# Kernel tuning notes

Hardware: AMD Instinct MI355X
Metric: run time of the kernel (lower is better)

## Reference

```python
import jax, jax.numpy as jnp
import numpy as np

B, N, D, H = 128, 197, 384, 1536  # batch, patches+CLS, embed_dim, hidden_dim


def _layer_norm(x, g, b, eps=1e-5):
    m = jnp.mean(x, axis=-1, keepdims=True)
    v = jnp.mean(jnp.square(x - m), axis=-1, keepdims=True)
    return (x - m) * jax.lax.rsqrt(v + eps) * g + b


def setup_inputs() -> dict:
    key = jax.random.key(0)
    ks = jax.random.split(key, 8)
    x = jax.random.normal(ks[0], (B, N, D), dtype=jnp.float32)
    # quantum circuit surrogates: orthogonal-style square matrices
    V = jax.random.normal(ks[1], (D, D), dtype=jnp.float32) / np.sqrt(D)
    W = jax.random.normal(ks[2], (D, D), dtype=jnp.float32) / np.sqrt(D)
    ln1_g = jnp.ones((D,), jnp.float32); ln1_b = jnp.zeros((D,), jnp.float32)
    ln2_g = jnp.ones((D,), jnp.float32); ln2_b = jnp.zeros((D,), jnp.float32)
    W1 = jax.random.normal(ks[3], (D, H), dtype=jnp.float32) / np.sqrt(D)
    b1 = jnp.zeros((H,), jnp.float32)
    W2 = jax.random.normal(ks[4], (H, D), dtype=jnp.float32) / np.sqrt(H)
    b2 = jnp.zeros((D,), jnp.float32)
    return {"x": x, "ln1_g": ln1_g, "ln1_b": ln1_b, "V": V, "W": W,
            "ln2_g": ln2_g, "ln2_b": ln2_b, "W1": W1, "b1": b1, "W2": W2, "b2": b2}


def reference(x, ln1_g, ln1_b, V, W, ln2_g, ln2_b, W1, b1, W2, b2):
    inp = _layer_norm(x, ln1_g, ln1_b)
    # normalization across the patch axis (dim=1), exactly as in the torch code
    inp = inp / jnp.sqrt(jnp.sum(jnp.square(inp) + 1e-4, axis=1, keepdims=True) + 1e-8)
    # Vx circuit: unary-basis probabilities |(V x_i)_d|^2 -> vx[b, d, i]
    vx = jnp.square(jnp.einsum('de,bne->bdn', V, inp))            # [B, D, N]
    # xWx circuit: (x_i^T W x_j)^2 -> xwx[b, i, j]
    y = jnp.einsum('bnd,de->bne', inp, W)                         # [B, N, D]
    xwx = jnp.square(jnp.einsum('bne,bme->bnm', y, inp))          # [B, N, N]
    vx = jnp.sqrt(vx + 1e-8)
    xwx = jnp.sqrt(xwx + 1e-8)
    attn = jax.nn.softmax(xwx, axis=-1)                           # [B, N, N]
    t = jnp.einsum('bnm,bdm->bnd', attn, vx)                      # attn @ vx^T
    x = x + t
    h = _layer_norm(x, ln2_g, ln2_b)
    h = jax.nn.gelu(h @ W1 + b1) @ W2 + b2                        # dropout=0 (eval)
    return x + h
```

## Files before the change

### kernel.cpp

```cpp
#include <hip/hip_runtime.h>
#include <math.h>

typedef unsigned short u16;
typedef unsigned int u32;
typedef __bf16 bfv8 __attribute__((ext_vector_type(8)));
typedef float f32x4 __attribute__((ext_vector_type(4)));

#define BB 128
#define NN 197
#define DD 384
#define HH 1536
#define BN (BB*NN)
#define NP 224

__device__ __forceinline__ float bf2f(u16 h){ u32 u = ((u32)h)<<16; float f; __builtin_memcpy(&f,&u,4); return f; }
__device__ __forceinline__ u16 f2bf(float x){ u32 u; __builtin_memcpy(&u,&x,4); u = (u + 0x7fffu + ((u>>16)&1u))>>16; return (u16)u; }

__device__ __forceinline__ float fast_gelu(float z){
  float t2 = 1.5957691216f*z*(1.f + 0.044715f*z*z);
  return z * __builtin_amdgcn_rcpf(1.f + __expf(-t2));
}

__device__ __forceinline__ void gload16(const void* g, void* s){
  __builtin_amdgcn_global_load_lds(
      (const __attribute__((address_space(1))) void*)g,
      (__attribute__((address_space(3))) void*)s, 16, 0, 0);
}

#define WAITV(N) asm volatile("s_waitcnt vmcnt(" #N ")" ::: "memory")

__global__ __launch_bounds__(256) void ln1_stats(const float* __restrict__ x,
    float* __restrict__ mu, float* __restrict__ rv){
  int row = blockIdx.x*4 + (threadIdx.x>>6);
  int lane = threadIdx.x & 63;
  const float* xr = x + (long)row*DD;
  float s=0.f, ss=0.f;
  #pragma unroll
  for (int j=0;j<DD/64;j++){ float v = xr[lane + j*64]; s+=v; ss+=v*v; }
  #pragma unroll
  for (int m=32;m;m>>=1){ s += __shfl_xor(s,m); ss += __shfl_xor(ss,m); }
  if (lane==0){
    float mn = s*(1.f/DD);
    float var = ss*(1.f/DD) - mn*mn;
    mu[row]=mn; rv[row]=1.f/sqrtf(var+1e-5f);
  }
}

__global__ __launch_bounds__(256) void colnorm(const float* __restrict__ x,
    const float* __restrict__ mu, const float* __restrict__ rv,
    const float* __restrict__ g, const float* __restrict__ bt,
    float* __restrict__ scale){
  int i = blockIdx.x*256 + threadIdx.x;
  int b = i/DD, d = i - b*DD;
  const float* xp = x + (long)b*NN*DD + d;
  float gd = g[d], bd = bt[d];
  float s = 0.f;
  for (int n=0;n<NN;n++){
    float v = (xp[(long)n*DD] - mu[b*NN+n]) * rv[b*NN+n] * gd + bd;
    s += v*v;
  }
  scale[i] = 1.f/sqrtf(s + 197.f*1e-4f + 1e-8f);
}

__global__ __launch_bounds__(256) void ln_apply(const float* __restrict__ x,
    const float* __restrict__ mu, const float* __restrict__ rv,
    const float* __restrict__ g, const float* __restrict__ bt,
    const float* __restrict__ scale, u16* __restrict__ inpn){
  long i = (long)blockIdx.x*256 + threadIdx.x;
  int d = (int)(i % DD);
  long row = i / DD;
  int b = (int)(row / NN);
  float v = (x[i]-mu[row])*rv[row]*g[d]+bt[d];
  inpn[i] = f2bf(v * scale[b*DD+d]);
}

__global__ __launch_bounds__(256) void prep_weights(const float* __restrict__ V, const float* __restrict__ W,
    const float* __restrict__ W1, const float* __restrict__ W2,
    u16* __restrict__ Vb, u16* __restrict__ Wt, u16* __restrict__ W1t, u16* __restrict__ W2t){
  int i = blockIdx.x*256 + threadIdx.x;
  if (i < DD*DD){
    Vb[i] = f2bf(V[i]);
    int r = i/DD, c = i - r*DD;
    Wt[c*DD + r] = f2bf(W[i]);
  }
  {
    int r = i/HH, c = i - r*HH;
    W1t[(long)c*DD + r] = f2bf(W1[i]);
    int r2 = i/DD, c2 = i - r2*DD;
    W2t[(long)c2*HH + r2] = f2bf(W2[i]);
  }
}

__global__ __launch_bounds__(256) void transpose_pad(const u16* __restrict__ U, u16* __restrict__ Ut){
  __shared__ u16 tile[32][33];
  int b = blockIdx.x, dt = blockIdx.y, pt = blockIdx.z;
  int tx = threadIdx.x & 31, ty = threadIdx.x >> 5;
  const u16* Ub = U + (long)b*NN*DD;
  #pragma unroll
  for (int j=0;j<4;j++){
    int p = pt*32 + ty + j*8;
    int d = dt*32 + tx;
    tile[ty+j*8][tx] = (p<NN) ? Ub[(long)p*DD + d] : (u16)0;
  }
  __syncthreads();
  u16* Utb = Ut + (long)b*DD*NP;
  #pragma unroll
  for (int j=0;j<4;j++){
    int d = dt*32 + ty + j*8;
    int p = pt*32 + tx;
    Utb[(long)d*NP + p] = tile[tx][ty+j*8];
  }
}

__global__ __launch_bounds__(256) void softmax_rows(const u16* __restrict__ S, u16* __restrict__ attn){
  int row = blockIdx.x*4 + (threadIdx.x>>6);
  int lane = threadIdx.x & 63;
  const u16* sr = S + (long)row*NP;
  float v[4]; float mx = -1e30f;
  #pragma unroll
  for (int j=0;j<4;j++){ int c = lane + j*64; v[j] = (c<NN)? bf2f(sr[c]) : -1e30f; mx = fmaxf(mx, v[j]); }
  #pragma unroll
  for (int m=32;m;m>>=1) mx = fmaxf(mx, __shfl_xor(mx,m));
  float sm = 0.f;
  #pragma unroll
  for (int j=0;j<4;j++){ v[j] = __expf(v[j]-mx); sm += v[j]; }
  #pragma unroll
  for (int m=32;m;m>>=1) sm += __shfl_xor(sm,m);
  float inv = __builtin_amdgcn_rcpf(sm);
  u16* ar = attn + (long)row*NP;
  #pragma unroll
  for (int j=0;j<4;j++){ int c = lane + j*64; if (c<NP) ar[c] = f2bf(v[j]*inv); }
}

__global__ __launch_bounds__(256) void ln2_fused(const u16* __restrict__ x2,
    const float* __restrict__ g, const float* __restrict__ bt, u16* __restrict__ h){
  int row = blockIdx.x*4 + (threadIdx.x>>6);
  int lane = threadIdx.x & 63;
  const u16* xr = x2 + (long)row*DD;
  float v[6]; float s=0.f, ss=0.f;
  #pragma unroll
  for (int j=0;j<6;j++){ v[j]=bf2f(xr[lane+j*64]); s+=v[j]; ss+=v[j]*v[j]; }
  #pragma unroll
  for (int m=32;m;m>>=1){ s+=__shfl_xor(s,m); ss+=__shfl_xor(ss,m); }
  float mn = s*(1.f/DD);
  float rvv = 1.f/sqrtf(ss*(1.f/DD)-mn*mn+1e-5f);
  u16* hr = h + (long)row*DD;
  #pragma unroll
  for (int j=0;j<6;j++){ int d = lane+j*64; hr[d] = f2bf((v[j]-mn)*rvv*g[d]+bt[d]); }
}

struct EpiS { u16* s;
  __device__ void operator()(int b, int r0, int c, const f32x4* col, int mf) const {
    u16* sp = s + ((long)b*NN + r0)*NP + c;
    for (int m=0;m<mf;m++)
      #pragma unroll
      for (int i=0;i<4;i++){
        int r = r0 + m*16 + i;
        float v = col[m][i];
        if (r < NN) sp[(long)(m*16+i)*NP] = f2bf(sqrtf(v*v + 1e-8f));
      }
  }};
struct EpiX2 { u16* x2; const float* x;
  __device__ void operator()(int b, int r0, int c, const f32x4* col, int mf) const {
    long base = ((long)b*NN + r0)*DD + c;
    for (int m=0;m<mf;m++)
      #pragma unroll
      for (int i=0;i<4;i++){
        int r = r0 + m*16 + i;
        if (r < NN){ long idx = base + (long)(m*16+i)*DD; x2[idx] = f2bf(x[idx] + col[m][i]); }
      }
  }};
struct EpiGelu { u16* g; const float* b1;
  __device__ void operator()(int, int r0, int c, const f32x4* col, int mf) const {
    float bb = b1[c];
    u16* gp = g + (long)r0*HH + c;
    for (int m=0;m<mf;m++)
      #pragma unroll
      for (int i=0;i<4;i++)
        gp[(long)(m*16+i)*HH] = f2bf(fast_gelu(col[m][i] + bb));
  }};
struct EpiOut { float* o; const u16* x2; const float* b2;
  __device__ void operator()(int, int r0, int c, const f32x4* col, int mf) const {
    float bb = b2[c];
    long base = (long)r0*DD + c;
    for (int m=0;m<mf;m++)
      #pragma unroll
      for (int i=0;i<4;i++){
        long idx = base + (long)(m*16+i)*DD;
        o[idx] = bf2f(x2[idx]) + col[m][i] + bb;
      }
  }};

template<int BM, class Epi>
__global__ __launch_bounds__(256) void gemm_nt(const u16* __restrict__ A, const u16* __restrict__ B,
    int M, int N, int K, int lda, int ldb, long sA, long sB, int NT, Epi epi)
{
  constexpr int MF = BM/32;
  constexpr int ALOADS = BM/64;
  __shared__ __align__(16) u16 As[2][BM*32];
  __shared__ __align__(16) u16 Bs[2][128*32];
  int wg;
  { int flat = blockIdx.x, nwg = gridDim.x;
    int xcd = flat & 7, local = flat >> 3;
    int q = nwg >> 3, r = nwg & 7;
    wg = (xcd < r ? xcd*(q+1) : r*(q+1) + (xcd-r)*q) + local; }
  const int bm = wg / NT, bn = wg - bm*NT;
  const int bat = blockIdx.y;
  const u16* Ab = A + (long)bat*sA;
  const u16* Bb = B + (long)bat*sB;
  const int t = threadIdx.x, lane = t&63, wid = t>>6, wr = wid>>1, wc = wid&1;
  const int row0 = bm*BM, col0 = bn*128;

  long aoff[ALOADS]; int asoff[ALOADS];
  #pragma unroll
  for (int i=0;i<ALOADS;i++){
    int ob = (i*256+t)*16;
    int r = ob>>6, ke = (ob&63)>>1;
    int ra = row0+r; if (ra>M-1) ra=M-1;
    aoff[i] = (long)ra*lda + ke; asoff[i] = ob;
  }
  long boff[2]; int bsoff[2];
  #pragma unroll
  for (int i=0;i<2;i++){
    int ob = (i*256+t)*16;
    int r = ob>>6, ke = (ob&63)>>1;
    int rb = col0+r; if (rb>N-1) rb=N-1;
    boff[i] = (long)rb*ldb + ke; bsoff[i] = ob;
  }

  auto stage = [&](int buf, int k0){
    #pragma unroll
    for (int i=0;i<ALOADS;i++) gload16(Ab + aoff[i] + k0, (char*)As[buf] + asoff[i]);
    #pragma unroll
    for (int i=0;i<2;i++)      gload16(Bb + boff[i] + k0, (char*)Bs[buf] + bsoff[i]);
  };

  f32x4 acc[MF][4] = {};
  const int kg = (lane>>4)*8, rl = lane&15;
  const int ntile = K/32;

  stage(0, 0);
  stage(1, 32);
  int buf = 0;
  for (int tt=0; tt<ntile; ++tt){
    if (tt+1 < ntile){
      if constexpr (ALOADS == 1) WAITV(3); else WAITV(4);
    } else {
      WAITV(0);
    }
    __builtin_amdgcn_sched_barrier(0);
    __builtin_amdgcn_s_barrier();

    bfv8 af[MF], bfr[4];
    #pragma unroll
    for (int m=0;m<MF;m++) af[m]  = *(const bfv8*)&As[buf][(wr*(BM/2) + m*16 + rl)*32 + kg];
    #pragma unroll
    for (int n=0;n<4;n++)  bfr[n] = *(const bfv8*)&Bs[buf][(wc*64 + n*16 + rl)*32 + kg];
    #pragma unroll
    for (int m=0;m<MF;m++)
      #pragma unroll
      for (int n=0;n<4;n++)
        acc[m][n] = __builtin_amdgcn_mfma_f32_16x16x32_bf16(af[m], bfr[n], acc[m][n], 0,0,0);

    __builtin_amdgcn_s_barrier();
    __builtin_amdgcn_sched_barrier(0);
    if (tt+2 < ntile) stage(buf, (tt+2)*32);
    buf ^= 1;
  }

  const int rbase = row0 + wr*(BM/2) + (lane>>4)*4;
  const int cbase = col0 + wc*64 + rl;
  #pragma unroll
  for (int n=0;n<4;n++){
    int c = cbase + n*16;
    if (c < N){
      f32x4 colv[MF];
      #pragma unroll
      for (int m=0;m<MF;m++) colv[m] = acc[m][n];
      epi(bat, rbase, c, colv, MF);
    }
  }
}

__global__ __launch_bounds__(256) void gemm12(const u16* __restrict__ A,
    const u16* __restrict__ B1, const u16* __restrict__ B2,
    u16* __restrict__ U, u16* __restrict__ Y)
{
  __shared__ __align__(16) u16 As[2][64*32];
  __shared__ __align__(16) u16 B1s[2][128*32];
  __shared__ __align__(16) u16 B2s[2][128*32];
  int wg;
  { int flat = blockIdx.x, nwg = gridDim.x;
    int xcd = flat & 7, local = flat >> 3;
    int q = nwg >> 3, r = nwg & 7;
    wg = (xcd < r ? xcd*(q+1) : r*(q+1) + (xcd-r)*q) + local; }
  const int bm = wg/3, bn = wg - bm*3;
  const int t = threadIdx.x, lane = t&63, wid = t>>6, wr = wid>>1, wc = wid&1;
  const int row0 = bm*64, col0 = bn*128;

  int ob = t*16, r = ob>>6, ke = (ob&63)>>1;
  long aoff = (long)(row0+r)*DD + ke;
  int asoff = ob;
  long boff[2]; int bsoff[2];
  #pragma unroll
  for (int i=0;i<2;i++){
    int ob2 = (i*256+t)*16, r2 = ob2>>6, ke2 = (ob2&63)>>1;
    boff[i] = (long)(col0+r2)*DD + ke2; bsoff[i] = ob2;
  }

  auto stage = [&](int buf, int k0){
    gload16(A + aoff + k0, (char*)As[buf] + asoff);
    #pragma unroll
    for (int i=0;i<2;i++){
      gload16(B1 + boff[i] + k0, (char*)B1s[buf] + bsoff[i]);
      gload16(B2 + boff[i] + k0, (char*)B2s[buf] + bsoff[i]);
    }
  };

  f32x4 acc1[2][4] = {}, acc2[2][4] = {};
  const int kg = (lane>>4)*8, rl = lane&15;

  stage(0, 0);
  stage(1, 32);
  int buf = 0;
  for (int tt=0; tt<12; ++tt){
    if (tt < 11) WAITV(5); else WAITV(0);
    __builtin_amdgcn_sched_barrier(0);
    __builtin_amdgcn_s_barrier();

    bfv8 af[2], b1r[4], b2r[4];
    #pragma unroll
    for (int m=0;m<2;m++) af[m] = *(const bfv8*)&As[buf][(wr*32 + m*16 + rl)*32 + kg];
    #pragma unroll
    for (int n=0;n<4;n++){
      b1r[n] = *(const bfv8*)&B1s[buf][(wc*64 + n*16 + rl)*32 + kg];
      b2r[n] = *(const bfv8*)&B2s[buf][(wc*64 + n*16 + rl)*32 + kg];
    }
    #pragma unroll
    for (int m=0;m<2;m++)
      #pragma unroll
      for (int n=0;n<4;n++){
        acc1[m][n] = __builtin_amdgcn_mfma_f32_16x16x32_bf16(af[m], b1r[n], acc1[m][n], 0,0,0);
        acc2[m][n] = __builtin_amdgcn_mfma_f32_16x16x32_bf16(af[m], b2r[n], acc2[m][n], 0,0,0);
      }

    __builtin_amdgcn_s_barrier();
    __builtin_amdgcn_sched_barrier(0);
    if (tt+2 < 12) stage(buf, (tt+2)*32);
    buf ^= 1;
  }

  const int rbase = row0 + wr*32 + (lane>>4)*4;
  const int cbase = col0 + wc*64 + rl;
  #pragma unroll
  for (int n=0;n<4;n++){
    int c = cbase + n*16;
    #pragma unroll
    for (int m=0;m<2;m++)
      #pragma unroll
      for (int i=0;i<4;i++){
        long idx = (long)(rbase + m*16 + i)*DD + c;
        float v1 = acc1[m][n][i];
        U[idx] = f2bf(sqrtf(v1*v1 + 1e-8f));
        Y[idx] = f2bf(acc2[m][n][i]);
      }
  }
}

extern "C" void kernel_launch(void* const* d_in, const int* in_sizes, int n_in,
                              void* d_out, int out_size, void* d_ws, size_t ws_size,
                              hipStream_t stream){
  const float* x     = (const float*)d_in[0];
  const float* g1    = (const float*)d_in[1];
  const float* b1n   = (const float*)d_in[2];
  const float* V     = (const float*)d_in[3];
  const float* W     = (const float*)d_in[4];
  const float* g2    = (const float*)d_in[5];
  const float* b2n   = (const float*)d_in[6];
  const float* W1    = (const float*)d_in[7];
  const float* bias1 = (const float*)d_in[8];
  const float* W2    = (const float*)d_in[9];
  const float* bias2 = (const float*)d_in[10];
  float* out = (float*)d_out;

  char* ws = (char*)d_ws;
  size_t off = 0;
  auto take = [&](size_t bytes)->char*{ char* p = ws + off; off += (bytes + 255) & ~(size_t)255; return p; };

  float* mu    = (float*)take((size_t)BN*4);
  float* rv    = (float*)take((size_t)BN*4);
  float* scale = (float*)take((size_t)BB*DD*4);
  char* aliasBase = ws + off;
  u16*  inpn = (u16*) take((size_t)BN*DD*2);
  u16*  U    = (u16*) take((size_t)BN*DD*2);
  u16*  Ut   = (u16*) take((size_t)BB*DD*NP*2);
  u16*  Yb   = (u16*) take((size_t)BN*DD*2);
  u16*  S    = (u16*) take((size_t)BN*NP*2);
  u16*  attn = (u16*) take((size_t)BN*NP*2);
  u16*  x2   = (u16*) take((size_t)BN*DD*2);
  u16*  h    = (u16*) take((size_t)BN*DD*2);
  u16*  Vb   = (u16*) take((size_t)DD*DD*2);
  u16*  Wt   = (u16*) take((size_t)DD*DD*2);
  u16*  W1t  = (u16*) take((size_t)DD*HH*2);
  u16*  W2t  = (u16*) take((size_t)DD*HH*2);
  u16*  G    = (u16*)aliasBase;

  prep_weights<<<DD*HH/256, 256, 0, stream>>>(V, W, W1, W2, Vb, Wt, W1t, W2t);
  ln1_stats  <<<BN/4,       256, 0, stream>>>(x, mu, rv);
  colnorm    <<<BB*DD/256,  256, 0, stream>>>(x, mu, rv, g1, b1n, scale);
  ln_apply   <<<BN*DD/256,  256, 0, stream>>>(x, mu, rv, g1, b1n, scale, inpn);

  gemm12<<<394*3, 256, 0, stream>>>(inpn, Vb, Wt, U, Yb);
  { dim3 grid(BB, DD/32, NP/32);
    transpose_pad<<<grid, 256, 0, stream>>>(U, Ut); }
  { dim3 grid(4*2, BB);
    gemm_nt<64,EpiS><<<grid,256,0,stream>>>(Yb, inpn, NN, NN, DD, DD, DD,
                                         (long)NN*DD, (long)NN*DD, 2, EpiS{S}); }
  softmax_rows<<<BN/4, 256, 0, stream>>>(S, attn);
  { dim3 grid(4*3, BB);
    gemm_nt<64,EpiX2><<<grid,256,0,stream>>>(attn, Ut, NN, DD, NP, NP, NP,
                                          (long)NN*NP, (long)DD*NP, 3, EpiX2{x2, x}); }
  ln2_fused<<<BN/4, 256, 0, stream>>>(x2, g2, b2n, h);
  { dim3 grid(197*12, 1);
    gemm_nt<128,EpiGelu><<<grid,256,0,stream>>>(h, W1t, BN, HH, DD, DD, DD, 0, 0, 12, EpiGelu{G, bias1}); }
  { dim3 grid(394*3, 1);
    gemm_nt<64,EpiOut><<<grid,256,0,stream>>>(G, W2t, BN, DD, HH, HH, HH, 0, 0, 3, EpiOut{out, x2, bias2}); }
}
```

Baseline: 395.1 us.

## Stage GELU GEMM output through LDS for coalesced stores; tile weight transposes

Adds a dedicated FC1 GEMM kernel that writes bias+GELU results into a 128x128 LDS tile and then stores them to global memory as 16-byte row-contiguous vectors. The previous epilogue wrote scattered 2-byte values with a row stride. The weight preparation is also split into a plain cast plus shared-memory tiled transpose kernels, so the transposed weight writes are coalesced. The extra 32KB of LDS per block may reduce occupancy, and the weight prep now takes several launches instead of one.

```diff
diff --git a/kernel.cpp b/kernel.cpp
--- a/kernel.cpp
+++ b/kernel.cpp
@@ -5,6 +5,7 @@
 typedef unsigned int u32;
 typedef __bf16 bfv8 __attribute__((ext_vector_type(8)));
 typedef float f32x4 __attribute__((ext_vector_type(4)));
+typedef u16 u16v8 __attribute__((ext_vector_type(8)));
 
 #define BB 128
 #define NN 197
@@ -74,21 +75,23 @@
   inpn[i] = f2bf(v * scale[b*DD+d]);
 }
 
-__global__ __launch_bounds__(256) void prep_weights(const float* __restrict__ V, const float* __restrict__ W,
-    const float* __restrict__ W1, const float* __restrict__ W2,
-    u16* __restrict__ Vb, u16* __restrict__ Wt, u16* __restrict__ W1t, u16* __restrict__ W2t){
+__global__ __launch_bounds__(256) void cast_bf16(const float* __restrict__ src, u16* __restrict__ dst, int n){
   int i = blockIdx.x*256 + threadIdx.x;
-  if (i < DD*DD){
-    Vb[i] = f2bf(V[i]);
-    int r = i/DD, c = i - r*DD;
-    Wt[c*DD + r] = f2bf(W[i]);
-  }
-  {
-    int r = i/HH, c = i - r*HH;
-    W1t[(long)c*DD + r] = f2bf(W1[i]);
-    int r2 = i/DD, c2 = i - r2*DD;
-    W2t[(long)c2*HH + r2] = f2bf(W2[i]);
-  }
+  if (i < n) dst[i] = f2bf(src[i]);
+}
+
+__global__ __launch_bounds__(256) void transpose_cast(const float* __restrict__ src, u16* __restrict__ dst,
+    int R, int C){
+  __shared__ float tile[32][33];
+  int rt = blockIdx.x, ct = blockIdx.y;
+  int tx = threadIdx.x & 31, ty = threadIdx.x >> 5;
+  #pragma unroll
+  for (int j=0;j<4;j++)
+    tile[ty+j*8][tx] = src[(long)(rt*32+ty+j*8)*C + ct*32+tx];
+  __syncthreads();
+  #pragma unroll
+  for (int j=0;j<4;j++)
+    dst[(long)(ct*32+ty+j*8)*R + rt*32+tx] = f2bf(tile[tx][ty+j*8]);
 }
 
 __global__ __launch_bounds__(256) void transpose_pad(const u16* __restrict__ U, u16* __restrict__ Ut){
@@ -169,15 +172,6 @@
         int r = r0 + m*16 + i;
         if (r < NN){ long idx = base + (long)(m*16+i)*DD; x2[idx] = f2bf(x[idx] + col[m][i]); }
       }
-  }};
-struct EpiGelu { u16* g; const float* b1;
-  __device__ void operator()(int, int r0, int c, const f32x4* col, int mf) const {
-    float bb = b1[c];
-    u16* gp = g + (long)r0*HH + c;
-    for (int m=0;m<mf;m++)
-      #pragma unroll
-      for (int i=0;i<4;i++)
-        gp[(long)(m*16+i)*HH] = f2bf(fast_gelu(col[m][i] + bb));
   }};
 struct EpiOut { float* o; const u16* x2; const float* b2;
   __device__ void operator()(int, int r0, int c, const f32x4* col, int mf) const {
@@ -282,6 +276,87 @@
   }
 }
 
+__global__ __launch_bounds__(256) void gemm5_coal(const u16* __restrict__ A, const u16* __restrict__ B,
+    const float* __restrict__ b1, u16* __restrict__ G)
+{
+  __shared__ __align__(16) u16 As[2][128*32];
+  __shared__ __align__(16) u16 Bs[2][128*32];
+  __shared__ __align__(16) u16 otile[128*128];
+  int wg;
+  { int flat = blockIdx.x, nwg = gridDim.x;
+    int xcd = flat & 7, local = flat >> 3;
+    int q = nwg >> 3, r = nwg & 7;
+    wg = (xcd < r ? xcd*(q+1) : r*(q+1) + (xcd-r)*q) + local; }
+  const int bm = wg / 12, bn = wg - bm*12;
+  const int t = threadIdx.x, lane = t&63, wid = t>>6, wr = wid>>1, wc = wid&1;
+  const int row0 = bm*128, col0 = bn*128;
+
+  long aoff[2], boff[2]; int soff[2];
+  #pragma unroll
+  for (int i=0;i<2;i++){
+    int ob = (i*256+t)*16;
+    int r = ob>>6, ke = (ob&63)>>1;
+    aoff[i] = (long)(row0+r)*DD + ke;
+    boff[i] = (long)(col0+r)*DD + ke;
+    soff[i] = ob;
+  }
+
+  auto stage = [&](int buf, int k0){
+    #pragma unroll
+    for (int i=0;i<2;i++){
+      gload16(A + aoff[i] + k0, (char*)As[buf] + soff[i]);
+      gload16(B + boff[i] + k0, (char*)Bs[buf] + soff[i]);
+    }
+  };
+
+  f32x4 acc[4][4] = {};
+  const int kg = (lane>>4)*8, rl = lane&15;
+
+  stage(0, 0);
+  stage(1, 32);
+  int buf = 0;
+  for (int tt=0; tt<12; ++tt){
+    if (tt < 11) WAITV(4); else WAITV(0);
+    __builtin_amdgcn_sched_barrier(0);
+    __builtin_amdgcn_s_barrier();
+
+    bfv8 af[4], bfr[4];
+    #pragma unroll
+    for (int m=0;m<4;m++) af[m]  = *(const bfv8*)&As[buf][(wr*64 + m*16 + rl)*32 + kg];
+    #pragma unroll
+    for (int n=0;n<4;n++) bfr[n] = *(const bfv8*)&Bs[buf][(wc*64 + n*16 + rl)*32 + kg];
+    #pragma unroll
+    for (int m=0;m<4;m++)
+      #pragma unroll
+      for (int n=0;n<4;n++)
+        acc[m][n] = __builtin_amdgcn_mfma_f32_16x16x32_bf16(af[m], bfr[n], acc[m][n], 0,0,0);
+
+    __builtin_amdgcn_s_barrier();
+    __builtin_amdgcn_sched_barrier(0);
+    if (tt+2 < 12) stage(buf, (tt+2)*32);
+    buf ^= 1;
+  }
+
+  const int rloc = wr*64 + (lane>>4)*4;
+  #pragma unroll
+  for (int n=0;n<4;n++){
+    int cl = wc*64 + n*16 + rl;
+    float bb = b1[col0 + cl];
+    #pragma unroll
+    for (int m=0;m<4;m++)
+      #pragma unroll
+      for (int i=0;i<4;i++)
+        otile[(rloc + m*16 + i)*128 + cl] = f2bf(fast_gelu(acc[m][n][i] + bb));
+  }
+  __syncthreads();
+  #pragma unroll
+  for (int k=0;k<8;k++){
+    int chunk = k*256 + t;
+    int row = chunk>>4, col8 = (chunk&15)*8;
+    *(u16v8*)(G + (long)(row0+row)*HH + col0 + col8) = *(const u16v8*)&otile[row*128 + col8];
+  }
+}
+
 __global__ __launch_bounds__(256) void gemm12(const u16* __restrict__ A,
     const u16* __restrict__ B1, const u16* __restrict__ B2,
     u16* __restrict__ U, u16* __restrict__ Y)
@@ -405,7 +480,10 @@
   u16*  W2t  = (u16*) take((size_t)DD*HH*2);
   u16*  G    = (u16*)aliasBase;
 
-  prep_weights<<<DD*HH/256, 256, 0, stream>>>(V, W, W1, W2, Vb, Wt, W1t, W2t);
+  cast_bf16<<<DD*DD/256, 256, 0, stream>>>(V, Vb, DD*DD);
+  { dim3 g(DD/32, DD/32); transpose_cast<<<g, 256, 0, stream>>>(W,  Wt,  DD, DD); }
+  { dim3 g(DD/32, HH/32); transpose_cast<<<g, 256, 0, stream>>>(W1, W1t, DD, HH); }
+  { dim3 g(HH/32, DD/32); transpose_cast<<<g, 256, 0, stream>>>(W2, W2t, HH, DD); }
   ln1_stats  <<<BN/4,       256, 0, stream>>>(x, mu, rv);
   colnorm    <<<BB*DD/256,  256, 0, stream>>>(x, mu, rv, g1, b1n, scale);
   ln_apply   <<<BN*DD/256,  256, 0, stream>>>(x, mu, rv, g1, b1n, scale, inpn);
@@ -421,8 +499,8 @@
     gemm_nt<64,EpiX2><<<grid,256,0,stream>>>(attn, Ut, NN, DD, NP, NP, NP,
                                           (long)NN*NP, (long)DD*NP, 3, EpiX2{x2, x}); }
   ln2_fused<<<BN/4, 256, 0, stream>>>(x2, g2, b2n, h);
-  { dim3 grid(197*12, 1);
-    gemm_nt<128,EpiGelu><<<grid,256,0,stream>>>(h, W1t, BN, HH, DD, DD, DD, 0, 0, 12, EpiGelu{G, bias1}); }
+  gemm5_coal<<<197*12, 256, 0, stream>>>(h, W1t, bias1, G);
   { dim3 grid(394*3, 1);
-    gemm_nt<64,EpiOut><<<grid,256,0,stream>>>(G, W2t, BN, DD, HH, HH, HH, 0, 0, 3, EpiOut{out, x2, bias2}); }
-}
+    gemm_nt<64,EpiOut><<<grid,256,0,stream>>>(G, W2t, BN, DD, HH, HH, HH, 0, 0, 3,
+                                          EpiOut{out, x2, bias2}); }
+}
```

New measurement: 394.7 us. Within noise of the previous version (-0.1%).
